# Kernel optimization log

Measured on AMD Instinct MI355X. Metric: run time of the kernel, lower is better.

## Reference

```python
import jax, jax.numpy as jnp
import numpy as np

N_NODES = 100000
N_EDGES = 1600000
HID = 256
HEADS = 4
HEAD_DIM = HID // HEADS
EPS = 1e-5


def _layernorm(x, g, b):
    mu = jnp.mean(x, axis=-1, keepdims=True)
    var = jnp.mean(jnp.square(x - mu), axis=-1, keepdims=True)
    return (x - mu) * jax.lax.rsqrt(var + EPS) * g + b


def setup_inputs() -> dict:
    key = jax.random.key(0)
    ks = jax.random.split(key, 16)
    s = 0.05  # small init, mimics xavier gain=0.1
    inp = {
        'h': jax.random.normal(ks[0], (N_NODES, HID), jnp.float32),
        'src': jax.random.randint(ks[1], (N_EDGES,), 0, N_NODES, jnp.int32),
        'dst': jax.random.randint(ks[2], (N_EDGES,), 0, N_NODES, jnp.int32),
        'Wq': jax.random.normal(ks[3], (HID, HID), jnp.float32) * s,
        'bq': jnp.zeros((HID,), jnp.float32),
        'Wk': jax.random.normal(ks[4], (HID, HID), jnp.float32) * s,
        'bk': jnp.zeros((HID,), jnp.float32),
        'Wv': jax.random.normal(ks[5], (HID, HID), jnp.float32) * s,
        'bv': jnp.zeros((HID,), jnp.float32),
        'Wo': jax.random.normal(ks[6], (HID, HID), jnp.float32) * s,
        'bo': jnp.zeros((HID,), jnp.float32),
        'W1': jax.random.normal(ks[7], (HID, 2 * HID), jnp.float32) * s,
        'b1': jnp.zeros((2 * HID,), jnp.float32),
        'W2': jax.random.normal(ks[8], (2 * HID, HID), jnp.float32) * s,
        'b2': jnp.zeros((HID,), jnp.float32),
        'g1': jnp.ones((HID,), jnp.float32),
        'be1': jnp.zeros((HID,), jnp.float32),
        'g2': jnp.ones((HID,), jnp.float32),
        'be2': jnp.zeros((HID,), jnp.float32),
    }
    return inp


def reference(h, src, dst, Wq, bq, Wk, bk, Wv, bv, Wo, bo, W1, b1, W2, b2, g1, be1, g2, be2):
    N = h.shape[0]
    scale = HEAD_DIM ** -0.5
    h_norm = _layernorm(h, g1, be1)
    Q = (h_norm @ Wq + bq).reshape(N, HEADS, HEAD_DIM)
    K = (h_norm @ Wk + bk).reshape(N, HEADS, HEAD_DIM)
    V = (h_norm @ Wv + bv).reshape(N, HEADS, HEAD_DIM)

    # per-edge attention logits: q from dst, k from src  -> [E, heads]
    logits = jnp.einsum('ehd,ehd->eh', Q[dst], K[src]) * scale

    # edge softmax grouped by destination node (dgl.ops.edge_softmax)
    seg_max = jax.ops.segment_max(logits, dst, num_segments=N)  # [N, heads]
    e = jnp.exp(logits - seg_max[dst])
    seg_sum = jax.ops.segment_sum(e, dst, num_segments=N)
    w = e / seg_sum[dst]  # [E, heads]

    # message = V[src] * attn ; aggregate by sum over incoming edges
    msg = V[src] * w[:, :, None]  # [E, heads, head_dim]
    h_new = jax.ops.segment_sum(msg, dst, num_segments=N).reshape(N, HID)

    h_attn = h_new @ Wo + bo
    h = h + h_attn  # dropout is identity in eval
    h2 = _layernorm(h, g2, be2)
    ffn = jax.nn.relu(h2 @ W1 + b1) @ W2 + b2
    return h + ffn
```

## Files before the change

kernel.cpp:

```cpp
#include <hip/hip_runtime.h>
#include <hip/hip_bf16.h>

#define NN 100000
#define NE 1600000

typedef __attribute__((ext_vector_type(8))) short bf16x8;
typedef __attribute__((ext_vector_type(4))) float f32x4;
typedef __attribute__((ext_vector_type(2))) float f32x2;
typedef __attribute__((ext_vector_type(2))) unsigned int u32x2;
typedef __attribute__((ext_vector_type(4))) unsigned int u32x4;

__device__ __forceinline__ float bf2f(unsigned short u) {
    union { unsigned int i; float f; } c; c.i = ((unsigned int)u) << 16; return c.f;
}
__device__ __forceinline__ unsigned short f2bf(float f) {
    union { float f; unsigned int i; } c; c.f = f;
    unsigned int lsb = (c.i >> 16) & 1u;
    c.i += 0x7FFFu + lsb;
    return (unsigned short)(c.i >> 16);
}
__device__ __forceinline__ u32x4 pack8bf(f32x4 a, f32x4 b) {
    u32x4 p;
    p.x = f2bf(a[0]) | ((unsigned int)f2bf(a[1]) << 16);
    p.y = f2bf(a[2]) | ((unsigned int)f2bf(a[3]) << 16);
    p.z = f2bf(b[0]) | ((unsigned int)f2bf(b[1]) << 16);
    p.w = f2bf(b[2]) | ((unsigned int)f2bf(b[3]) << 16);
    return p;
}
__device__ __forceinline__ unsigned int pack4fp8(f32x4 v) {
    unsigned int w = __builtin_amdgcn_cvt_pk_fp8_f32(v[0], v[1], 0, false);
    return __builtin_amdgcn_cvt_pk_fp8_f32(v[2], v[3], w, true);
}
__device__ __forceinline__ void gload_lds16(const void* g, void* l) {
    __builtin_amdgcn_global_load_lds(
        (const __attribute__((address_space(1))) void*)g,
        (__attribute__((address_space(3))) void*)l, 16, 0, 0);
}

__global__ __launch_bounds__(256) void ln_k(
    const float* __restrict__ x, const float* __restrict__ g,
    const float* __restrict__ b, unsigned short* __restrict__ y, int nrows)
{
    int w = threadIdx.x >> 6, lane = threadIdx.x & 63;
    int row = blockIdx.x * 4 + w;
    if (row >= nrows) return;
    const float4 xv = *(const float4*)(x + (size_t)row * 256 + lane * 4);
    float s  = xv.x + xv.y + xv.z + xv.w;
    float sq = xv.x*xv.x + xv.y*xv.y + xv.z*xv.z + xv.w*xv.w;
    #pragma unroll
    for (int m = 1; m < 64; m <<= 1) {
        s  += __shfl_xor(s,  m);
        sq += __shfl_xor(sq, m);
    }
    float mu  = s * (1.0f / 256.0f);
    float var = sq * (1.0f / 256.0f) - mu * mu;
    float r = rsqrtf(var + 1e-5f);
    float4 gv = *(const float4*)(g + lane * 4);
    float4 bv = *(const float4*)(b + lane * 4);
    ushort4 o;
    o.x = f2bf((xv.x - mu) * r * gv.x + bv.x);
    o.y = f2bf((xv.y - mu) * r * gv.y + bv.y);
    o.z = f2bf((xv.z - mu) * r * gv.z + bv.z);
    o.w = f2bf((xv.w - mu) * r * gv.w + bv.w);
    *(ushort4*)(y + (size_t)row * 256 + lane * 4) = o;
}

__global__ __launch_bounds__(256) void wcv_all_k(
    const float* __restrict__ Wq, const float* __restrict__ Wk, const float* __restrict__ Wv,
    const float* __restrict__ Wo, const float* __restrict__ W1, const float* __restrict__ W2,
    unsigned short* __restrict__ Wqkvt, unsigned short* __restrict__ Wot,
    unsigned short* __restrict__ W1t, unsigned short* __restrict__ W2t,
    const float* __restrict__ bq, const float* __restrict__ bk, const float* __restrict__ bv,
    float* __restrict__ bqkv)
{
    int id = blockIdx.x;
    int t = threadIdx.x;
    if (id == 512) {
        bqkv[t] = bq[t]; bqkv[256 + t] = bk[t]; bqkv[512 + t] = bv[t];
        return;
    }
    const float* W; unsigned short* Wt; int K, N, kx, ny;
    if (id < 192) {
        int grp = id >> 6, l = id & 63;
        W = (grp == 0) ? Wq : ((grp == 1) ? Wk : Wv);
        Wt = Wqkvt + grp * 256 * 256;
        K = 256; N = 256; kx = l & 7; ny = l >> 3;
    } else if (id < 256) {
        int l = id - 192; W = Wo; Wt = Wot; K = 256; N = 256; kx = l & 7; ny = l >> 3;
    } else if (id < 384) {
        int l = id - 256; W = W1; Wt = W1t; K = 256; N = 512; kx = l & 7; ny = l >> 3;
    } else {
        int l = id - 384; W = W2; Wt = W2t; K = 512; N = 256; kx = l & 15; ny = l >> 4;
    }
    __shared__ unsigned short tl[32][33];
    int bk2 = kx * 32, bn = ny * 32;
    int lx = t & 31, ly = t >> 5;
    #pragma unroll
    for (int r = 0; r < 32; r += 8)
        tl[ly + r][lx] = f2bf(W[(size_t)(bk2 + ly + r) * N + bn + lx]);
    __syncthreads();
    #pragma unroll
    for (int r = 0; r < 32; r += 8)
        Wt[(size_t)(bn + ly + r) * K + bk2 + lx] = tl[lx][ly + r];
}

template<int NBX, int OMODE, bool RELU, bool RES>
__global__ __launch_bounds__(512) void mgemm_k(
    const unsigned short* __restrict__ A, const unsigned short* __restrict__ Wt,
    const float* __restrict__ bias, void* __restrict__ outv, void* __restrict__ out2,
    const void* __restrict__ res, const float* __restrict__ g, const float* __restrict__ be,
    int M, int N, int K)
{
    __shared__ __align__(16) char lds[73728];
    const int t = threadIdx.x;
    const int lane = t & 63;
    const int wid = t >> 6;
    const int wm = wid >> 2, wn = wid & 3;

    int bmi, bni;
    if (NBX > 0) {
        const int nwg = gridDim.x;
        const int q = nwg >> 3, r = nwg & 7;
        const int xcd = blockIdx.x & 7, idx = blockIdx.x >> 3;
        const int wgid = (xcd < r) ? (xcd * (q + 1) + idx)
                                   : (r * (q + 1) + (xcd - r) * q + idx);
        bmi = wgid / NBX; bni = wgid - bmi * NBX;
    } else {
        bmi = blockIdx.y; bni = blockIdx.x;
    }
    const int bm = bmi * 128, bn = bni * 256;

    f32x4 acc[4][4] = {};

    const int ra_s = t >> 2;
    const int sa_s = (t & 3) ^ (ra_s & 3);
    const size_t arow = (size_t)min(bm + ra_s, M - 1) * K + sa_s * 8;
    const int rb0 = t >> 2;
    const int sb0 = (t & 3) ^ (rb0 & 3);
    const int rb1 = (512 + t) >> 2;
    const int sb1 = (t & 3) ^ (rb1 & 3);
    const size_t brow0 = (size_t)(bn + rb0) * K + sb0 * 8;
    const size_t brow1 = (size_t)(bn + rb1) * K + sb1 * 8;

    const int fr = lane & 15, fs = lane >> 4;
    const int rslot = fs ^ (fr & 3);

    const int KS = K >> 5;

#define STAGE(b, k0) { \
        unsigned short* Ab = (unsigned short*)(lds + (b) * 8192); \
        unsigned short* Bb = (unsigned short*)(lds + 24576 + (b) * 16384); \
        const int kk_ = (k0) << 5; \
        gload_lds16(A + arow + kk_, Ab + t * 8); \
        gload_lds16(Wt + brow0 + kk_, Bb + t * 8); \
        gload_lds16(Wt + brow1 + kk_, Bb + (512 + t) * 8); }

    STAGE(0, 0)
    STAGE(1, 1)
    int cur = 0;
    for (int ks = 0; ks < KS; ++ks) {
        if (ks + 1 < KS) asm volatile("s_waitcnt vmcnt(3)" ::: "memory");
        else             asm volatile("s_waitcnt vmcnt(0)" ::: "memory");
        __builtin_amdgcn_s_barrier();
        if (ks + 2 < KS) {
            int nb = cur + 2; if (nb >= 3) nb -= 3;
            STAGE(nb, ks + 2)
        }
        const unsigned short* As = (const unsigned short*)(lds + cur * 8192);
        const unsigned short* Bs = (const unsigned short*)(lds + 24576 + cur * 16384);
        bf16x8 af[4], bf[4];
        #pragma unroll
        for (int fm = 0; fm < 4; ++fm)
            af[fm] = *(const bf16x8*)&As[(wm * 64 + fm * 16 + fr) * 32 + rslot * 8];
        #pragma unroll
        for (int fn = 0; fn < 4; ++fn)
            bf[fn] = *(const bf16x8*)&Bs[(wn * 64 + fn * 16 + fr) * 32 + rslot * 8];
        #pragma unroll
        for (int fm = 0; fm < 4; ++fm)
            #pragma unroll
            for (int fn = 0; fn < 4; ++fn)
                acc[fm][fn] = __builtin_amdgcn_mfma_f32_16x16x32_bf16(
                    af[fm], bf[fn], acc[fm][fn], 0, 0, 0);
        if (++cur == 3) cur = 0;
    }
#undef STAGE
    __syncthreads();

    float* wl = (float*)(lds + wid * 4352);
    float* stats = (float*)(lds + 34816);
    const int rr = lane >> 2;
    const int c4 = (lane & 3) * 16;
    const int qg = lane >> 4;

    #pragma unroll
    for (int fm = 0; fm < 4; ++fm) {
        #pragma unroll
        for (int fn = 0; fn < 4; ++fn)
            #pragma unroll
            for (int i = 0; i < 4; ++i)
                wl[(qg * 4 + i) * 68 + fn * 16 + fr] = acc[fm][fn][i];
        f32x4 v0 = *(const f32x4*)&wl[rr * 68 + c4 + 0];
        f32x4 v1 = *(const f32x4*)&wl[rr * 68 + c4 + 4];
        f32x4 v2 = *(const f32x4*)&wl[rr * 68 + c4 + 8];
        f32x4 v3 = *(const f32x4*)&wl[rr * 68 + c4 + 12];
        const int rowg = bm + wm * 64 + fm * 16 + rr;
        const int colg = bn + wn * 64 + c4;
        if (rowg < M) {
            v0 += *(const f32x4*)&bias[colg + 0];
            v1 += *(const f32x4*)&bias[colg + 4];
            v2 += *(const f32x4*)&bias[colg + 8];
            v3 += *(const f32x4*)&bias[colg + 12];
            if (RES) {
                if (OMODE == 4) {
                    const unsigned short* rp = (const unsigned short*)res + (size_t)rowg * N + colg;
                    u32x4 ra = *(const u32x4*)rp;
                    u32x4 rb = *(const u32x4*)(rp + 8);
                    v0[0] += bf2f(ra.x & 0xffff); v0[1] += bf2f(ra.x >> 16);
                    v0[2] += bf2f(ra.y & 0xffff); v0[3] += bf2f(ra.y >> 16);
                    v1[0] += bf2f(ra.z & 0xffff); v1[1] += bf2f(ra.z >> 16);
                    v1[2] += bf2f(ra.w & 0xffff); v1[3] += bf2f(ra.w >> 16);
                    v2[0] += bf2f(rb.x & 0xffff); v2[1] += bf2f(rb.x >> 16);
                    v2[2] += bf2f(rb.y & 0xffff); v2[3] += bf2f(rb.y >> 16);
                    v3[0] += bf2f(rb.z & 0xffff); v3[1] += bf2f(rb.z >> 16);
                    v3[2] += bf2f(rb.w & 0xffff); v3[3] += bf2f(rb.w >> 16);
                } else {
                    const float* rp = (const float*)res + (size_t)rowg * N + colg;
                    v0 += *(const f32x4*)(rp + 0);
                    v1 += *(const f32x4*)(rp + 4);
                    v2 += *(const f32x4*)(rp + 8);
                    v3 += *(const f32x4*)(rp + 12);
                }
            }
            if (RELU) {
                #pragma unroll
                for (int j = 0; j < 4; ++j) {
                    v0[j] = fmaxf(v0[j], 0.f); v1[j] = fmaxf(v1[j], 0.f);
                    v2[j] = fmaxf(v2[j], 0.f); v3[j] = fmaxf(v3[j], 0.f);
                }
            }
        } else {
            v0 = 0.f; v1 = 0.f; v2 = 0.f; v3 = 0.f;
        }

        if (OMODE == 3) {
            acc[fm][0] = v0; acc[fm][1] = v1; acc[fm][2] = v2; acc[fm][3] = v3;
        } else if (rowg < M) {
            if (OMODE == 0 || OMODE == 4) {
                float* op = (float*)outv + (size_t)rowg * N + colg;
                *(f32x4*)(op + 0) = v0; *(f32x4*)(op + 4) = v1;
                *(f32x4*)(op + 8) = v2; *(f32x4*)(op + 12) = v3;
            } else if (OMODE == 1) {
                unsigned short* op = (unsigned short*)outv + (size_t)rowg * N + colg;
                *(u32x4*)(op + 0) = pack8bf(v0, v1);
                *(u32x4*)(op + 8) = pack8bf(v2, v3);
            } else {
                if (colg < 256) {
                    unsigned short* op = (unsigned short*)outv + (size_t)rowg * 256 + colg;
                    *(u32x4*)(op + 0) = pack8bf(v0, v1);
                    *(u32x4*)(op + 8) = pack8bf(v2, v3);
                } else {
                    u32x4 p8;
                    p8.x = pack4fp8(v0); p8.y = pack4fp8(v1);
                    p8.z = pack4fp8(v2); p8.w = pack4fp8(v3);
                    *(u32x4*)((unsigned char*)out2 + (size_t)rowg * 512 + (colg - 256)) = p8;
                }
            }
        }
    }

    if (OMODE == 3) {
        #pragma unroll
        for (int fm = 0; fm < 4; ++fm) {
            float s = 0.f, q = 0.f;
            #pragma unroll
            for (int j = 0; j < 4; ++j)
                #pragma unroll
                for (int c = 0; c < 4; ++c) {
                    float x = acc[fm][j][c];
                    s += x; q += x * x;
                }
            s += __shfl_xor(s, 1); q += __shfl_xor(q, 1);
            s += __shfl_xor(s, 2); q += __shfl_xor(q, 2);
            if ((lane & 3) == 0) {
                int rowl = wm * 64 + fm * 16 + rr;
                stats[rowl * 8 + wn * 2 + 0] = s;
                stats[rowl * 8 + wn * 2 + 1] = q;
            }
        }
        __syncthreads();
        #pragma unroll
        for (int fm = 0; fm < 4; ++fm) {
            const int rowl = wm * 64 + fm * 16 + rr;
            const int rowg = bm + rowl;
            float s = stats[rowl * 8 + 0] + stats[rowl * 8 + 2] + stats[rowl * 8 + 4] + stats[rowl * 8 + 6];
            float q = stats[rowl * 8 + 1] + stats[rowl * 8 + 3] + stats[rowl * 8 + 5] + stats[rowl * 8 + 7];
            float mu = s * (1.0f / 256.0f);
            float var = q * (1.0f / 256.0f) - mu * mu;
            float rstd = rsqrtf(var + 1e-5f);
            const int colg = bn + wn * 64 + c4;
            if (rowg < M) {
                unsigned short* mp = (unsigned short*)out2 + (size_t)rowg * 256 + colg;
                *(u32x4*)(mp + 0) = pack8bf(acc[fm][0], acc[fm][1]);
                *(u32x4*)(mp + 8) = pack8bf(acc[fm][2], acc[fm][3]);
                f32x4 nv[4];
                #pragma unroll
                for (int j = 0; j < 4; ++j) {
                    f32x4 gv = *(const f32x4*)&g[colg + j * 4];
                    f32x4 bv = *(const f32x4*)&be[colg + j * 4];
                    #pragma unroll
                    for (int c = 0; c < 4; ++c)
                        nv[j][c] = (acc[fm][j][c] - mu) * rstd * gv[c] + bv[c];
                }
                unsigned short* op = (unsigned short*)outv + (size_t)rowg * 256 + colg;
                *(u32x4*)(op + 0) = pack8bf(nv[0], nv[1]);
                *(u32x4*)(op + 8) = pack8bf(nv[2], nv[3]);
            }
        }
    }
}

__global__ void degcnt_k(const int* __restrict__ dst, int* __restrict__ deg, int E)
{
    int e = blockIdx.x * blockDim.x + threadIdx.x;
    if (e < E) atomicAdd(deg + dst[e], 1);
}

__global__ __launch_bounds__(1024) void scanA_k(int* __restrict__ a, int* __restrict__ aux, int n)
{
    __shared__ int wsum[16];
    __shared__ int wpre[16];
    int t = threadIdx.x, lane = t & 63, w = t >> 6;
    int i = blockIdx.x * 1024 + t;
    int v = (i < n) ? a[i] : 0;
    int s = v;
    #pragma unroll
    for (int d = 1; d < 64; d <<= 1) {
        int u = __shfl_up(s, d);
        if (lane >= d) s += u;
    }
    if (lane == 63) wsum[w] = s;
    __syncthreads();
    if (t == 0) {
        int run = 0;
        #pragma unroll
        for (int j = 0; j < 16; ++j) { wpre[j] = run; run += wsum[j]; }
        aux[blockIdx.x] = run;
    }
    __syncthreads();
    if (i < n) a[i] = wpre[w] + s - v;
}

__global__ __launch_bounds__(128) void scanB_k(int* __restrict__ aux, int* __restrict__ tot, int nb)
{
    __shared__ int ws[2];
    int t = threadIdx.x, lane = t & 63, w = t >> 6;
    int v = (t < nb) ? aux[t] : 0;
    int s = v;
    #pragma unroll
    for (int d = 1; d < 64; d <<= 1) {
        int u = __shfl_up(s, d);
        if (lane >= d) s += u;
    }
    if (lane == 63) ws[w] = s;
    __syncthreads();
    int add = (w == 1) ? ws[0] : 0;
    if (t < nb) aux[t] = add + s - v;
    if (t == nb - 1) tot[0] = add + s;
}

__global__ __launch_bounds__(1024) void scanC_k(int* __restrict__ a, const int* __restrict__ aux, int n)
{
    int i = blockIdx.x * 1024 + threadIdx.x;
    if (i < n) a[i] += aux[blockIdx.x];
}

__global__ void scatter_k(
    const int* __restrict__ dst, const int* __restrict__ srcarr,
    const int* __restrict__ off, int* __restrict__ cursor,
    int* __restrict__ csr, int E)
{
    int e = blockIdx.x * blockDim.x + threadIdx.x;
    if (e >= E) return;
    int d = dst[e];
    int pos = off[d] + atomicAdd(cursor + d, 1);
    csr[pos] = srcarr[e];
}

__global__ __launch_bounds__(256) void attn_k(
    const int* __restrict__ csr, const int* __restrict__ off,
    const unsigned short* __restrict__ Q, const unsigned char* __restrict__ KV8,
    unsigned short* __restrict__ hnew)
{
    int w = threadIdx.x >> 6, lane = threadIdx.x & 63;
    int n = blockIdx.x * 4 + w;
    if (n >= NN) return;
    int e0 = off[n], e1 = off[n + 1];

    u32x2 qr = __builtin_nontemporal_load((const u32x2*)(Q + (size_t)n * 256 + lane * 4));
    const float q0 = bf2f((unsigned short)(qr.x & 0xffff)) * 0.125f;
    const float q1 = bf2f((unsigned short)(qr.x >> 16))    * 0.125f;
    const float q2 = bf2f((unsigned short)(qr.y & 0xffff)) * 0.125f;
    const float q3 = bf2f((unsigned short)(qr.y >> 16))    * 0.125f;

    float s = 0.f;
    float a0 = 0.f, a1 = 0.f, a2 = 0.f, a3 = 0.f;

    int i = e0;
    for (; i + 7 < e1; i += 8) {
        int ns[8];
        #pragma unroll
        for (int j = 0; j < 8; ++j) ns[j] = csr[i + j];
        unsigned int kd[8], vd[8];
        #pragma unroll
        for (int j = 0; j < 8; ++j) {
            const unsigned char* r = KV8 + (size_t)ns[j] * 512 + lane * 4;
            kd[j] = *(const unsigned int*)r;
            vd[j] = *(const unsigned int*)(r + 256);
        }
        float l[8];
        #pragma unroll
        for (int j = 0; j < 8; ++j) {
            f32x2 ka = __builtin_amdgcn_cvt_pk_f32_fp8(kd[j], false);
            f32x2 kb = __builtin_amdgcn_cvt_pk_f32_fp8(kd[j], true);
            l[j] = q0 * ka.x + q1 * ka.y + q2 * kb.x + q3 * kb.y;
        }
        #pragma unroll
        for (int m2 = 1; m2 < 16; m2 <<= 1) {
            #pragma unroll
            for (int j = 0; j < 8; ++j) l[j] += __shfl_xor(l[j], m2);
        }
        #pragma unroll
        for (int j = 0; j < 8; ++j) {
            float p = __expf(l[j]);
            f32x2 va = __builtin_amdgcn_cvt_pk_f32_fp8(vd[j], false);
            f32x2 vb = __builtin_amdgcn_cvt_pk_f32_fp8(vd[j], true);
            s  += p;
            a0 += p * va.x; a1 += p * va.y;
            a2 += p * vb.x; a3 += p * vb.y;
        }
    }
    for (; i + 3 < e1; i += 4) {
        int ns[4];
        #pragma unroll
        for (int j = 0; j < 4; ++j) ns[j] = csr[i + j];
        unsigned int kd[4], vd[4];
        #pragma unroll
        for (int j = 0; j < 4; ++j) {
            const unsigned char* r = KV8 + (size_t)ns[j] * 512 + lane * 4;
            kd[j] = *(const unsigned int*)r;
            vd[j] = *(const unsigned int*)(r + 256);
        }
        float l[4];
        #pragma unroll
        for (int j = 0; j < 4; ++j) {
            f32x2 ka = __builtin_amdgcn_cvt_pk_f32_fp8(kd[j], false);
            f32x2 kb = __builtin_amdgcn_cvt_pk_f32_fp8(kd[j], true);
            l[j] = q0 * ka.x + q1 * ka.y + q2 * kb.x + q3 * kb.y;
        }
        #pragma unroll
        for (int m2 = 1; m2 < 16; m2 <<= 1) {
            #pragma unroll
            for (int j = 0; j < 4; ++j) l[j] += __shfl_xor(l[j], m2);
        }
        #pragma unroll
        for (int j = 0; j < 4; ++j) {
            float p = __expf(l[j]);
            f32x2 va = __builtin_amdgcn_cvt_pk_f32_fp8(vd[j], false);
            f32x2 vb = __builtin_amdgcn_cvt_pk_f32_fp8(vd[j], true);
            s  += p;
            a0 += p * va.x; a1 += p * va.y;
            a2 += p * vb.x; a3 += p * vb.y;
        }
    }
    for (; i < e1; ++i) {
        int n0 = csr[i];
        const unsigned char* r = KV8 + (size_t)n0 * 512 + lane * 4;
        unsigned int kd = *(const unsigned int*)r;
        unsigned int vd = *(const unsigned int*)(r + 256);
        f32x2 ka = __builtin_amdgcn_cvt_pk_f32_fp8(kd, false);
        f32x2 kb = __builtin_amdgcn_cvt_pk_f32_fp8(kd, true);
        float l0 = q0 * ka.x + q1 * ka.y + q2 * kb.x + q3 * kb.y;
        #pragma unroll
        for (int m2 = 1; m2 < 16; m2 <<= 1) l0 += __shfl_xor(l0, m2);
        float p = __expf(l0);
        f32x2 va = __builtin_amdgcn_cvt_pk_f32_fp8(vd, false);
        f32x2 vb = __builtin_amdgcn_cvt_pk_f32_fp8(vd, true);
        s  += p;
        a0 += p * va.x; a1 += p * va.y;
        a2 += p * vb.x; a3 += p * vb.y;
    }
    float inv = (e1 > e0) ? 1.0f / s : 0.f;
    u32x2 ov;
    ov.x = ((unsigned int)f2bf(a1 * inv) << 16) | f2bf(a0 * inv);
    ov.y = ((unsigned int)f2bf(a3 * inv) << 16) | f2bf(a2 * inv);
    __builtin_nontemporal_store(ov, (u32x2*)(hnew + (size_t)n * 256 + lane * 4));
}

extern "C" void kernel_launch(void* const* d_in, const int* in_sizes, int n_in,
                              void* d_out, int out_size, void* d_ws, size_t ws_size,
                              hipStream_t stream)
{
    if (n_in < 19) return;
    const float* h   = (const float*)d_in[0];
    const int*   src = (const int*)d_in[1];
    const int*   dst = (const int*)d_in[2];
    const float* Wq  = (const float*)d_in[3];
    const float* bq  = (const float*)d_in[4];
    const float* Wk  = (const float*)d_in[5];
    const float* bk  = (const float*)d_in[6];
    const float* Wv  = (const float*)d_in[7];
    const float* bv  = (const float*)d_in[8];
    const float* Wo  = (const float*)d_in[9];
    const float* bo  = (const float*)d_in[10];
    const float* W1  = (const float*)d_in[11];
    const float* b1  = (const float*)d_in[12];
    const float* W2  = (const float*)d_in[13];
    const float* b2  = (const float*)d_in[14];
    const float* g1  = (const float*)d_in[15];
    const float* be1 = (const float*)d_in[16];
    const float* g2  = (const float*)d_in[17];
    const float* be2 = (const float*)d_in[18];
    float* out = (float*)d_out;

    char* w = (char*)d_ws;
    unsigned short* hnormb = (unsigned short*)(w + 0);
    unsigned short* Qb     = (unsigned short*)(w + 51200000);
    unsigned char*  KV8    = (unsigned char*)(w + 102400000);
    int*            degoff = (int*)(w + 153600000);
    int*            cursor = (int*)(w + 154000384);
    int*            csr    = (int*)(w + 154400768);
    unsigned short* Wqkvt  = (unsigned short*)(w + 204800000);
    unsigned short* Wot    = (unsigned short*)(w + 205193216);
    unsigned short* W1t    = (unsigned short*)(w + 205324288);
    unsigned short* W2t    = (unsigned short*)(w + 205586432);
    float*          bqkv   = (float*)(w + 205848576);
    int*            scanaux= (int*)(w + 205851648);
    unsigned short* hnewb  = hnormb;
    unsigned short* h2nb   = hnormb;
    unsigned short* hmidb  = Qb;
    unsigned short* ffnmid = (unsigned short*)(w + 102400000);

    hipMemsetAsync(degoff, 0, 400384, stream);
    hipMemsetAsync(cursor, 0, 400384, stream);

    const int M = NN;
    dim3 blk(256);
    dim3 blk512(512);
    const int MB = (M + 127) / 128;
    const int SCAN_BLKS = (NN + 1023) / 1024;

    wcv_all_k<<<dim3(513), blk, 0, stream>>>(Wq, Wk, Wv, Wo, W1, W2,
                                             Wqkvt, Wot, W1t, W2t, bq, bk, bv, bqkv);

    degcnt_k<<<dim3((NE + 255) / 256), blk, 0, stream>>>(dst, degoff, NE);
    scanA_k<<<dim3(SCAN_BLKS), dim3(1024), 0, stream>>>(degoff, scanaux, NN);
    scanB_k<<<dim3(1), dim3(128), 0, stream>>>(scanaux, degoff + NN, SCAN_BLKS);
    scanC_k<<<dim3(SCAN_BLKS), dim3(1024), 0, stream>>>(degoff, scanaux, NN);
    scatter_k<<<dim3((NE + 255) / 256), blk, 0, stream>>>(dst, src, degoff, cursor, csr, NE);

    ln_k<<<dim3((NN + 3) / 4), blk, 0, stream>>>(h, g1, be1, hnormb, NN);

    mgemm_k<3, 2, false, false><<<dim3(3 * MB), blk512, 0, stream>>>(
        hnormb, Wqkvt, bqkv, Qb, KV8, nullptr, nullptr, nullptr, M, 768, 256);

    attn_k<<<dim3((NN + 3) / 4), blk, 0, stream>>>(csr, degoff, Qb, KV8, hnewb);

    dim3 go(1, MB);
    mgemm_k<0, 3, false, true><<<go, blk512, 0, stream>>>(
        hnewb, Wot, bo, h2nb, hmidb, h, g2, be2, M, 256, 256);

    mgemm_k<2, 1, true, false><<<dim3(2 * MB), blk512, 0, stream>>>(
        h2nb, W1t, b1, ffnmid, nullptr, nullptr, nullptr, nullptr, M, 512, 256);
    mgemm_k<0, 4, false, true><<<go, blk512, 0, stream>>>(
        ffnmid, W2t, b2, out, nullptr, hmidb, nullptr, nullptr, M, 256, 512);
}
```

Before: 579.2 us.

## Split wavefront into two half-waves processing alternate edges in attention kernel

The attention aggregation kernel now has each half of the 64-lane wave handle alternate incoming edges, with each lane loading 8 fp8 K/V values (8-byte loads) instead of 4. This halves the shuffle reduction depth per edge and uses packed f32x2 math plus exp2 with log2e folded into the query scale. A final cross-half shuffle combines the partial sums. It aims to cut shuffle and loop overhead and raise bytes per load in the gather. In exchange it adds a merge step, and nodes with an odd edge count leave one half-wave idle on the last edge.

```diff
diff --git a/kernel.cpp b/kernel.cpp
--- a/kernel.cpp
+++ b/kernel.cpp
@@ -395,105 +395,93 @@
     int n = blockIdx.x * 4 + w;
     if (n >= NN) return;
     int e0 = off[n], e1 = off[n + 1];
-
-    u32x2 qr = __builtin_nontemporal_load((const u32x2*)(Q + (size_t)n * 256 + lane * 4));
-    const float q0 = bf2f((unsigned short)(qr.x & 0xffff)) * 0.125f;
-    const float q1 = bf2f((unsigned short)(qr.x >> 16))    * 0.125f;
-    const float q2 = bf2f((unsigned short)(qr.y & 0xffff)) * 0.125f;
-    const float q3 = bf2f((unsigned short)(qr.y >> 16))    * 0.125f;
-
+    int hl = lane & 31, par = lane >> 5;
+
+    const float qs = 0.125f * 1.4426950408889634f;
+    f32x2 q01, q23, q45, q67;
+    {
+        u32x4 qa = __builtin_nontemporal_load((const u32x4*)(Q + (size_t)n * 256 + hl * 8));
+        q01[0] = bf2f((unsigned short)(qa.x & 0xffff)) * qs;
+        q01[1] = bf2f((unsigned short)(qa.x >> 16)) * qs;
+        q23[0] = bf2f((unsigned short)(qa.y & 0xffff)) * qs;
+        q23[1] = bf2f((unsigned short)(qa.y >> 16)) * qs;
+        q45[0] = bf2f((unsigned short)(qa.z & 0xffff)) * qs;
+        q45[1] = bf2f((unsigned short)(qa.z >> 16)) * qs;
+        q67[0] = bf2f((unsigned short)(qa.w & 0xffff)) * qs;
+        q67[1] = bf2f((unsigned short)(qa.w >> 16)) * qs;
+    }
+    f32x2 a01 = {0.f, 0.f}, a23 = {0.f, 0.f}, a45 = {0.f, 0.f}, a67 = {0.f, 0.f};
     float s = 0.f;
-    float a0 = 0.f, a1 = 0.f, a2 = 0.f, a3 = 0.f;
+    const unsigned char* KVl = KV8 + hl * 8;
 
     int i = e0;
     for (; i + 7 < e1; i += 8) {
-        int ns[8];
-        #pragma unroll
-        for (int j = 0; j < 8; ++j) ns[j] = csr[i + j];
-        unsigned int kd[8], vd[8];
-        #pragma unroll
-        for (int j = 0; j < 8; ++j) {
-            const unsigned char* r = KV8 + (size_t)ns[j] * 512 + lane * 4;
-            kd[j] = *(const unsigned int*)r;
-            vd[j] = *(const unsigned int*)(r + 256);
-        }
-        float l[8];
-        #pragma unroll
-        for (int j = 0; j < 8; ++j) {
-            f32x2 ka = __builtin_amdgcn_cvt_pk_f32_fp8(kd[j], false);
-            f32x2 kb = __builtin_amdgcn_cvt_pk_f32_fp8(kd[j], true);
-            l[j] = q0 * ka.x + q1 * ka.y + q2 * kb.x + q3 * kb.y;
-        }
-        #pragma unroll
-        for (int m2 = 1; m2 < 16; m2 <<= 1) {
-            #pragma unroll
-            for (int j = 0; j < 8; ++j) l[j] += __shfl_xor(l[j], m2);
-        }
-        #pragma unroll
-        for (int j = 0; j < 8; ++j) {
-            float p = __expf(l[j]);
-            f32x2 va = __builtin_amdgcn_cvt_pk_f32_fp8(vd[j], false);
-            f32x2 vb = __builtin_amdgcn_cvt_pk_f32_fp8(vd[j], true);
-            s  += p;
-            a0 += p * va.x; a1 += p * va.y;
-            a2 += p * vb.x; a3 += p * vb.y;
-        }
-    }
-    for (; i + 3 < e1; i += 4) {
-        int ns[4];
-        #pragma unroll
-        for (int j = 0; j < 4; ++j) ns[j] = csr[i + j];
-        unsigned int kd[4], vd[4];
-        #pragma unroll
-        for (int j = 0; j < 4; ++j) {
-            const unsigned char* r = KV8 + (size_t)ns[j] * 512 + lane * 4;
-            kd[j] = *(const unsigned int*)r;
-            vd[j] = *(const unsigned int*)(r + 256);
-        }
-        float l[4];
-        #pragma unroll
-        for (int j = 0; j < 4; ++j) {
-            f32x2 ka = __builtin_amdgcn_cvt_pk_f32_fp8(kd[j], false);
-            f32x2 kb = __builtin_amdgcn_cvt_pk_f32_fp8(kd[j], true);
-            l[j] = q0 * ka.x + q1 * ka.y + q2 * kb.x + q3 * kb.y;
-        }
-        #pragma unroll
-        for (int m2 = 1; m2 < 16; m2 <<= 1) {
-            #pragma unroll
-            for (int j = 0; j < 4; ++j) l[j] += __shfl_xor(l[j], m2);
-        }
-        #pragma unroll
-        for (int j = 0; j < 4; ++j) {
-            float p = __expf(l[j]);
-            f32x2 va = __builtin_amdgcn_cvt_pk_f32_fp8(vd[j], false);
-            f32x2 vb = __builtin_amdgcn_cvt_pk_f32_fp8(vd[j], true);
-            s  += p;
-            a0 += p * va.x; a1 += p * va.y;
-            a2 += p * vb.x; a3 += p * vb.y;
-        }
-    }
-    for (; i < e1; ++i) {
-        int n0 = csr[i];
-        const unsigned char* r = KV8 + (size_t)n0 * 512 + lane * 4;
-        unsigned int kd = *(const unsigned int*)r;
-        unsigned int vd = *(const unsigned int*)(r + 256);
-        f32x2 ka = __builtin_amdgcn_cvt_pk_f32_fp8(kd, false);
-        f32x2 kb = __builtin_amdgcn_cvt_pk_f32_fp8(kd, true);
-        float l0 = q0 * ka.x + q1 * ka.y + q2 * kb.x + q3 * kb.y;
-        #pragma unroll
-        for (int m2 = 1; m2 < 16; m2 <<= 1) l0 += __shfl_xor(l0, m2);
-        float p = __expf(l0);
-        f32x2 va = __builtin_amdgcn_cvt_pk_f32_fp8(vd, false);
-        f32x2 vb = __builtin_amdgcn_cvt_pk_f32_fp8(vd, true);
-        s  += p;
-        a0 += p * va.x; a1 += p * va.y;
-        a2 += p * vb.x; a3 += p * vb.y;
-    }
+        int b[4];
+        #pragma unroll
+        for (int t2 = 0; t2 < 4; ++t2) b[t2] = csr[i + 2 * t2 + par] << 9;
+        u32x2 kd[4], vd[4];
+        #pragma unroll
+        for (int t2 = 0; t2 < 4; ++t2) {
+            kd[t2] = *(const u32x2*)(KVl + (unsigned)b[t2]);
+            vd[t2] = *(const u32x2*)(KVl + (unsigned)b[t2] + 256);
+        }
+        #pragma unroll
+        for (int t2 = 0; t2 < 4; ++t2) {
+            f32x2 lv = q01 * __builtin_amdgcn_cvt_pk_f32_fp8(kd[t2].x, false);
+            lv += q23 * __builtin_amdgcn_cvt_pk_f32_fp8(kd[t2].x, true);
+            lv += q45 * __builtin_amdgcn_cvt_pk_f32_fp8(kd[t2].y, false);
+            lv += q67 * __builtin_amdgcn_cvt_pk_f32_fp8(kd[t2].y, true);
+            float l = lv[0] + lv[1];
+            l += __shfl_xor(l, 1);
+            l += __shfl_xor(l, 2);
+            l += __shfl_xor(l, 4);
+            float p = exp2f(l);
+            s += p;
+            f32x2 pp = {p, p};
+            a01 += pp * __builtin_amdgcn_cvt_pk_f32_fp8(vd[t2].x, false);
+            a23 += pp * __builtin_amdgcn_cvt_pk_f32_fp8(vd[t2].x, true);
+            a45 += pp * __builtin_amdgcn_cvt_pk_f32_fp8(vd[t2].y, false);
+            a67 += pp * __builtin_amdgcn_cvt_pk_f32_fp8(vd[t2].y, true);
+        }
+    }
+    for (; i < e1; i += 2) {
+        int eidx = i + par;
+        int idx = (eidx < e1) ? eidx : (e1 - 1);
+        int b = csr[idx] << 9;
+        u32x2 kd = *(const u32x2*)(KVl + (unsigned)b);
+        u32x2 vd = *(const u32x2*)(KVl + (unsigned)b + 256);
+        f32x2 lv = q01 * __builtin_amdgcn_cvt_pk_f32_fp8(kd.x, false);
+        lv += q23 * __builtin_amdgcn_cvt_pk_f32_fp8(kd.x, true);
+        lv += q45 * __builtin_amdgcn_cvt_pk_f32_fp8(kd.y, false);
+        lv += q67 * __builtin_amdgcn_cvt_pk_f32_fp8(kd.y, true);
+        float l = lv[0] + lv[1];
+        l += __shfl_xor(l, 1);
+        l += __shfl_xor(l, 2);
+        l += __shfl_xor(l, 4);
+        float p = (eidx < e1) ? exp2f(l) : 0.f;
+        s += p;
+        f32x2 pp = {p, p};
+        a01 += pp * __builtin_amdgcn_cvt_pk_f32_fp8(vd.x, false);
+        a23 += pp * __builtin_amdgcn_cvt_pk_f32_fp8(vd.x, true);
+        a45 += pp * __builtin_amdgcn_cvt_pk_f32_fp8(vd.y, false);
+        a67 += pp * __builtin_amdgcn_cvt_pk_f32_fp8(vd.y, true);
+    }
+
+    a01[0] += __shfl_xor(a01[0], 32); a01[1] += __shfl_xor(a01[1], 32);
+    a23[0] += __shfl_xor(a23[0], 32); a23[1] += __shfl_xor(a23[1], 32);
+    a45[0] += __shfl_xor(a45[0], 32); a45[1] += __shfl_xor(a45[1], 32);
+    a67[0] += __shfl_xor(a67[0], 32); a67[1] += __shfl_xor(a67[1], 32);
+    s += __shfl_xor(s, 32);
+
     float inv = (e1 > e0) ? 1.0f / s : 0.f;
-    u32x2 ov;
-    ov.x = ((unsigned int)f2bf(a1 * inv) << 16) | f2bf(a0 * inv);
-    ov.y = ((unsigned int)f2bf(a3 * inv) << 16) | f2bf(a2 * inv);
-    __builtin_nontemporal_store(ov, (u32x2*)(hnew + (size_t)n * 256 + lane * 4));
+    if (par == 0) {
+        u32x4 ov;
+        ov.x = f2bf(a01[0] * inv) | ((unsigned int)f2bf(a01[1] * inv) << 16);
+        ov.y = f2bf(a23[0] * inv) | ((unsigned int)f2bf(a23[1] * inv) << 16);
+        ov.z = f2bf(a45[0] * inv) | ((unsigned int)f2bf(a45[1] * inv) << 16);
+        ov.w = f2bf(a67[0] * inv) | ((unsigned int)f2bf(a67[1] * inv) << 16);
+        __builtin_nontemporal_store(ov, (u32x4*)(hnew + (size_t)n * 256 + hl * 8));
+    }
 }
 
 extern "C" void kernel_launch(void* const* d_in, const int* in_sizes, int n_in,
```

After: 580.9 us. About the same (+0.3%).
